# Kernel tuning notes

Measured on AMD Instinct MI355X. Metric: run time of the kernel, lower is better.

## Reference

```python
import jax, jax.numpy as jnp
import numpy as np

H = 512  # hidden_size


def _gru_gates(gi, gh, h):
    # gi, gh: [B, 3H] in PyTorch gate order (r, z, n)
    i_r, i_z, i_n = jnp.split(gi, 3, axis=-1)
    h_r, h_z, h_n = jnp.split(gh, 3, axis=-1)
    r = jax.nn.sigmoid(i_r + h_r)
    z = jax.nn.sigmoid(i_z + h_z)
    n = jnp.tanh(i_n + r * h_n)
    return (1.0 - z) * n + z * h


def _gru_layer(x, Wih, Whh, bih, bhh):
    # x: [B, T, in] -> outputs [B, T, H]; PyTorch nn.GRU math, h0 = 0
    gi = jnp.einsum('bti,gi->btg', x, Wih) + bih  # [B,T,3H], precompute input projections
    def step(h, gi_t):
        gh = h @ Whh.T + bhh
        h_new = _gru_gates(gi_t, gh, h)
        return h_new, h_new
    h0 = jnp.zeros((x.shape[0], H), dtype=x.dtype)
    _, hs = jax.lax.scan(step, h0, jnp.swapaxes(gi, 0, 1))
    return jnp.swapaxes(hs, 0, 1)


def _uniform_param(key, shape, fan):
    bound = 1.0 / np.sqrt(fan)
    return jax.random.uniform(key, shape, jnp.float32, -bound, bound)


def setup_inputs() -> dict:
    key = jax.random.key(0)
    ks = jax.random.split(key, 24)
    input_size, tf, B, T, horizon = 8, 8, 512, 336, 48
    inp = {
        'src': jax.random.normal(ks[0], (B, T, input_size), jnp.float32),
        'future_time_features': jax.random.normal(ks[1], (B, horizon, tf), jnp.float32),
        # encoder GRU layer 0
        'enc_Wih0': _uniform_param(ks[2], (3 * H, input_size), H),
        'enc_Whh0': _uniform_param(ks[3], (3 * H, H), H),
        'enc_bih0': _uniform_param(ks[4], (3 * H,), H),
        'enc_bhh0': _uniform_param(ks[5], (3 * H,), H),
        # encoder GRU layer 1
        'enc_Wih1': _uniform_param(ks[6], (3 * H, H), H),
        'enc_Whh1': _uniform_param(ks[7], (3 * H, H), H),
        'enc_bih1': _uniform_param(ks[8], (3 * H,), H),
        'enc_bhh1': _uniform_param(ks[9], (3 * H,), H),
        # dec0 Linear(H, H)
        'dec0_W': _uniform_param(ks[10], (H, H), H),
        'dec0_b': _uniform_param(ks[11], (H,), H),
        # decoder GRUCell(1 + tf, H)
        'cell_Wih': _uniform_param(ks[12], (3 * H, 1 + tf), H),
        'cell_Whh': _uniform_param(ks[13], (3 * H, H), H),
        'cell_bih': _uniform_param(ks[14], (3 * H,), H),
        'cell_bhh': _uniform_param(ks[15], (3 * H,), H),
        # fc Linear(H, 1)
        'fc_W': _uniform_param(ks[16], (1, H), H),
        'fc_b': _uniform_param(ks[17], (1,), H),
    }
    return inp


def reference(src, future_time_features,
              enc_Wih0, enc_Whh0, enc_bih0, enc_bhh0,
              enc_Wih1, enc_Whh1, enc_bih1, enc_bhh1,
              dec0_W, dec0_b, cell_Wih, cell_Whh, cell_bih, cell_bhh,
              fc_W, fc_b):
    # ---- encoder: 2-layer GRU, batch_first ----
    h1 = _gru_layer(src, enc_Wih0, enc_Whh0, enc_bih0, enc_bhh0)
    states = _gru_layer(h1, enc_Wih1, enc_Whh1, enc_bih1, enc_bhh1)  # [B,T,H]

    last_value = src[:, -1, 0:1]                      # [B,1]
    hidden = states[:, -1, :] @ dec0_W.T + dec0_b     # [B,H]

    tf_steps = jnp.swapaxes(future_time_features, 0, 1)  # [horizon,B,tf]

    def dec_step(carry, tf_t):
        hidden, last_value = carry
        x = jnp.concatenate([last_value, tf_t], axis=1)  # [B,1+tf]
        gi = x @ cell_Wih.T + cell_bih
        gh = hidden @ cell_Whh.T + cell_bhh
        hidden = _gru_gates(gi, gh, hidden)
        pred = hidden @ fc_W.T + fc_b                    # [B,1]
        return (hidden, pred), pred

    _, preds = jax.lax.scan(dec_step, (hidden, last_value), tf_steps)
    return jnp.swapaxes(preds, 0, 1)  # [B,horizon,1]
```

## Files before the change

### kernel.cpp

```cpp
#include <hip/hip_runtime.h>
#include <math.h>

typedef _Float16 half_t;
typedef _Float16 half8 __attribute__((ext_vector_type(8)));
typedef float floatx16 __attribute__((ext_vector_type(16)));
typedef unsigned int uint;

#define HD 512
#define BB 512
#define TT 336
#define HOR 48
#define NBLOCK 256
#define NTHREAD 512
#define GBLK 32
#define MFMA16(a,b,c) __builtin_amdgcn_mfma_f32_32x32x16_f16(a, b, c, 0, 0, 0)

__device__ __forceinline__ float sig_(float x) { return 1.0f / (1.0f + __expf(-x)); }

__global__ __launch_bounds__(256)
void prep_w2(const float* __restrict__ W1, const float* __restrict__ W2,
             half_t* __restrict__ D, int NKC, int NG)
{
    const int t = blockIdx.x * 256 + threadIdx.x;
    if (t >= 16 * NG * NKC * 64) return;
    const int lane = t & 63;
    const int kc = (t >> 6) % NKC;
    const int jtg = (t >> 6) / NKC;
    const int g = jtg % NG, jt = jtg / NG;
    const int row = g * 512 + jt * 32 + (lane & 31);
    const int k = kc * 16 + (lane >> 5) * 8;
    const float* Wp = (k < 512) ? W1 : W2;
    const int kk = (k < 512) ? k : (k - 512);
    const float4 lo = *(const float4*)(Wp + (size_t)row * 512 + kk);
    const float4 hi = *(const float4*)(Wp + (size_t)row * 512 + kk + 4);
    half8 h;
    h[0] = (half_t)lo.x; h[1] = (half_t)lo.y; h[2] = (half_t)lo.z; h[3] = (half_t)lo.w;
    h[4] = (half_t)hi.x; h[5] = (half_t)hi.y; h[6] = (half_t)hi.z; h[7] = (half_t)hi.w;
    *(half8*)(D + (size_t)t * 8) = h;
}

__global__ void lv_init_kernel(const float* __restrict__ src,
                               const float* __restrict__ fcb,
                               float* __restrict__ lvarr)
{
    const int b = threadIdx.x + blockIdx.x * blockDim.x;
    if (b < BB) lvarr[b] = src[((size_t)b * TT + (TT - 1)) * 8] - fcb[0];
}

struct PP {
    const half_t *BL0, *BWih1, *BWhh1, *Bcwhh, *Blin;
    half_t *h0f[2], *h1f[2], *hdf[2];
    float *hd32row;
    const float *src, *tff, *Wih0;
    const float *bih0, *bhh0, *bih1, *bhh1, *dec0b, *cWih, *cbih, *cbhh, *fcW, *fcb;
    float *lvarr, *out;
    uint *bars;
    int *tickets;
};

__device__ __forceinline__ uint aload_u(const uint* p) {
    return __hip_atomic_load(p, __ATOMIC_RELAXED, __HIP_MEMORY_SCOPE_AGENT);
}
__device__ __forceinline__ float aload_f(const float* p) {
    return __int_as_float(__hip_atomic_load((const int*)p, __ATOMIC_RELAXED, __HIP_MEMORY_SCOPE_AGENT));
}

__device__ __forceinline__ void xcd_barrier(uint* w)
{
    __syncthreads();
    if (threadIdx.x == 0) {
        const uint old = atomicAdd(w, 1u);
        const uint g0 = old >> 8;
        if ((old & 255u) == GBLK - 1) {
            __hip_atomic_store(w, (g0 + 1) << 8, __ATOMIC_RELAXED, __HIP_MEMORY_SCOPE_AGENT);
        } else {
            while ((aload_u(w) >> 8) == g0) __builtin_amdgcn_s_sleep(4);
        }
    }
    asm volatile("buffer_inv sc0" ::: "memory");
    __syncthreads();
}

__device__ __forceinline__ void dump_acc(float* red, int wv, int jl, int hi, const floatx16& a)
{
    #pragma unroll
    for (int rg = 0; rg < 16; ++rg)
        red[wv * 1024 + ((rg & 3) + 8 * (rg >> 2) + 4 * hi) * 32 + jl] = a[rg];
}
__device__ __forceinline__ void sum4(const float* red, int q, int jc, float* o)
{
    #pragma unroll
    for (int c = 0; c < 4; ++c) {
        const int ra = q * 4 + c, mi = ra >> 5, base = (ra & 31) * 32 + jc;
        o[c] = red[(0 + mi) * 1024 + base] + red[(2 + mi) * 1024 + base]
             + red[(4 + mi) * 1024 + base] + red[(6 + mi) * 1024 + base];
    }
}
__device__ __forceinline__ void sum22(const float* red, int q, int jc, float* lo, float* ho)
{
    #pragma unroll
    for (int c = 0; c < 4; ++c) {
        const int ra = q * 4 + c, mi = ra >> 5, base = (ra & 31) * 32 + jc;
        lo[c] = red[(0 + mi) * 1024 + base] + red[(2 + mi) * 1024 + base];
        ho[c] = red[(4 + mi) * 1024 + base] + red[(6 + mi) * 1024 + base];
    }
}

__device__ __forceinline__ void load_wlds(half_t* wlds, const half_t* Bsrc, int tid)
{
    #pragma unroll
    for (int it = 0; it < 12; ++it) {
        const int e = it * 512 + tid;
        const int gg = e >> 11, kc = (e >> 6) & 31, ln = e & 63;
        const int jj = ln & 31, h2 = ln >> 5;
        const half8 v = *(const half8*)(Bsrc + (size_t)e * 8);
        *(half8*)&wlds[(size_t)(gg * 32 + jj) * 512 + ((kc * 16 + h2 * 8) ^ ((jj & 15) << 3))] = v;
    }
}

__global__ __launch_bounds__(NTHREAD, 2)
void rnn_persist(PP p)
{
    __shared__ half_t wlds[3 * 32 * 512];
    __shared__ float  red[8 * 1024];
    __shared__ int    meta[2];
    __shared__ float  lvsh[64];

    const int tid = threadIdx.x;
    if (tid == 0) {
        int xcc;
        asm volatile("s_getreg_b32 %0, hwreg(HW_REG_XCC_ID)" : "=s"(xcc));
        xcc &= 7;
        meta[0] = xcc;
        meta[1] = atomicAdd(p.tickets + xcc, 1);
    }
    __syncthreads();
    const int g = meta[0];
    const int role = meta[1] & 31;
    const int L = role >> 4, jt = role & 15;

    const int wv = tid >> 6, lane = tid & 63;
    const int jl = lane & 31, hi = lane >> 5;
    const int mi = wv & 1, kh = wv >> 1;
    const int q = tid >> 5, jcell = tid & 31;
    const int row0g = g * 64;
    const int j = jt * 32 + jcell;
    const int swz16 = (jl & 15) << 3;
    const int gbase = g * 32768;
    const int joff = (j >> 4) * 512 + ((j >> 3) & 1) * 256 + (j & 7);

    uint* bword = p.bars + (size_t)g * 256;

    load_wlds(wlds, (L ? p.BWhh1 : p.BL0) + (size_t)jt * 6144 * 8, tid);

    const float* bi = L ? p.bih1 : p.bih0;
    const float* bh = L ? p.bhh1 : p.bhh0;
    const float bir = bi[j] + bh[j];
    const float biz = bi[512 + j] + bh[512 + j];
    const float bin = bi[1024 + j];
    const float bhn = bh[1024 + j];
    float w0r[8], w0z[8], w0n[8];
    if (!L) {
        #pragma unroll
        for (int i = 0; i < 8; ++i) {
            w0r[i] = p.Wih0[(size_t)j * 8 + i];
            w0z[i] = p.Wih0[(size_t)(512 + j) * 8 + i];
            w0n[i] = p.Wih0[(size_t)(1024 + j) * 8 + i];
        }
    }
    float hp[4] = {0.f, 0.f, 0.f, 0.f};

    for (int s = 0; s <= TT; ++s) {
        if (!L && s < TT) {
            floatx16 ar = {}, az = {}, an = {};
            const half_t* A = p.h0f[s & 1] + (size_t)(((g * 2 + mi) * 32 + kh * 8) * 64 + lane) * 8;
            #pragma unroll
            for (int kc = 0; kc < 8; ++kc) {
                const half8 a = *(const half8*)(A + kc * 512);
                const int ko = (kh * 128 + kc * 16 + hi * 8) ^ swz16;
                ar = MFMA16(a, *(const half8*)&wlds[(size_t)(0 * 32 + jl) * 512 + ko], ar);
                az = MFMA16(a, *(const half8*)&wlds[(size_t)(1 * 32 + jl) * 512 + ko], az);
                an = MFMA16(a, *(const half8*)&wlds[(size_t)(2 * 32 + jl) * 512 + ko], an);
            }
            float gr[4], gz[4], gn[4];
            dump_acc(red, wv, jl, hi, ar); __syncthreads(); sum4(red, q, jcell, gr); __syncthreads();
            dump_acc(red, wv, jl, hi, az); __syncthreads(); sum4(red, q, jcell, gz); __syncthreads();
            dump_acc(red, wv, jl, hi, an); __syncthreads(); sum4(red, q, jcell, gn);

            half_t* hofr = p.h0f[(s + 1) & 1];
            #pragma unroll
            for (int c = 0; c < 4; ++c) {
                const int r = q * 4 + c;
                const int br = row0g + r;
                const float* sp = p.src + ((size_t)br * TT + s) * 8;
                float xr = gr[c] + bir, xz = gz[c] + biz, xn = bin;
                #pragma unroll
                for (int i = 0; i < 8; ++i) {
                    const float xi = sp[i];
                    xr = fmaf(xi, w0r[i], xr);
                    xz = fmaf(xi, w0z[i], xz);
                    xn = fmaf(xi, w0n[i], xn);
                }
                const float rr = sig_(xr), zz = sig_(xz);
                const float nn = tanhf(xn + rr * (gn[c] + bhn));
                const float h = (1.f - zz) * nn + zz * hp[c];
                hp[c] = h;
                hofr[gbase + (r >> 5) * 16384 + (r & 31) * 8 + joff] = (half_t)h;
            }
        } else if (L && s >= 1) {
            floatx16 ar = {}, az = {}, an = {};
            if (kh < 2) {
                const half_t* A = p.h0f[s & 1] + (size_t)(((g * 2 + mi) * 32 + kh * 16) * 64 + lane) * 8;
                const half_t* Bb = p.BWih1 + ((size_t)jt * 6144 + kh * 1024 + lane) * 8;
                #pragma unroll 8
                for (int kc = 0; kc < 16; ++kc) {
                    const half8 a  = *(const half8*)(A + kc * 512);
                    const half8 u0 = *(const half8*)(Bb + (size_t)kc * 512);
                    const half8 u1 = *(const half8*)(Bb + (size_t)kc * 512 + 16384);
                    const half8 u2 = *(const half8*)(Bb + (size_t)kc * 512 + 32768);
                    ar = MFMA16(a, u0, ar);
                    az = MFMA16(a, u1, az);
                    an = MFMA16(a, u2, an);
                }
            } else {
                const half_t* A = p.h1f[s & 1] + (size_t)(((g * 2 + mi) * 32 + (kh - 2) * 16) * 64 + lane) * 8;
                #pragma unroll
                for (int kc = 0; kc < 16; ++kc) {
                    const half8 a = *(const half8*)(A + kc * 512);
                    const int ko = ((kh - 2) * 256 + kc * 16 + hi * 8) ^ swz16;
                    ar = MFMA16(a, *(const half8*)&wlds[(size_t)(0 * 32 + jl) * 512 + ko], ar);
                    az = MFMA16(a, *(const half8*)&wlds[(size_t)(1 * 32 + jl) * 512 + ko], az);
                    an = MFMA16(a, *(const half8*)&wlds[(size_t)(2 * 32 + jl) * 512 + ko], an);
                }
            }
            float gr[4], gz[4], gnl[4], gnh[4];
            dump_acc(red, wv, jl, hi, ar); __syncthreads(); sum4(red, q, jcell, gr); __syncthreads();
            dump_acc(red, wv, jl, hi, az); __syncthreads(); sum4(red, q, jcell, gz); __syncthreads();
            dump_acc(red, wv, jl, hi, an); __syncthreads(); sum22(red, q, jcell, gnl, gnh);

            half_t* hofr = p.h1f[(s + 1) & 1];
            #pragma unroll
            for (int c = 0; c < 4; ++c) {
                const int r = q * 4 + c;
                const float rr = sig_(gr[c] + bir), zz = sig_(gz[c] + biz);
                const float nn = tanhf(gnl[c] + bin + rr * (gnh[c] + bhn));
                const float h = (1.f - zz) * nn + zz * hp[c];
                hp[c] = h;
                hofr[gbase + (r >> 5) * 16384 + (r & 31) * 8 + joff] = (half_t)h;
            }
        }
        xcd_barrier(bword);
    }

    if (!L) {
        load_wlds(wlds, p.Bcwhh + (size_t)jt * 6144 * 8, tid);
    } else {
        floatx16 a0 = {};
        const half_t* A = p.h1f[1] + (size_t)(((g * 2 + mi) * 32 + kh * 8) * 64 + lane) * 8;
        const half_t* Bb = p.Blin + ((size_t)jt * 2048 + kh * 512 + lane) * 8;
        #pragma unroll
        for (int kc = 0; kc < 8; ++kc) {
            const half8 a = *(const half8*)(A + kc * 512);
            const half8 w = *(const half8*)(Bb + (size_t)kc * 512);
            a0 = MFMA16(a, w, a0);
        }
        float hv[4];
        dump_acc(red, wv, jl, hi, a0); __syncthreads(); sum4(red, q, jcell, hv);
        const float bj = p.dec0b[j];
        #pragma unroll
        for (int c = 0; c < 4; ++c) {
            const int r = q * 4 + c;
            const float h = hv[c] + bj;
            p.hd32row[(size_t)(row0g + r) * 512 + j] = h;
            p.hdf[0][gbase + (r >> 5) * 16384 + (r & 31) * 8 + joff] = (half_t)h;
        }
    }
    xcd_barrier(bword);

    float wR[9], wZ[9], wN[9];
    float dbr = 0.f, dbz = 0.f, dbn = 0.f, dbhn = 0.f, fw = 0.f, f0 = 0.f;
    if (!L) {
        #pragma unroll
        for (int i = 0; i < 9; ++i) {
            wR[i] = p.cWih[(size_t)j * 9 + i];
            wZ[i] = p.cWih[(size_t)(512 + j) * 9 + i];
            wN[i] = p.cWih[(size_t)(1024 + j) * 9 + i];
        }
        dbr = p.cbih[j] + p.cbhh[j];
        dbz = p.cbih[512 + j] + p.cbhh[512 + j];
        dbn = p.cbih[1024 + j];
        dbhn = p.cbhh[1024 + j];
        fw = p.fcW[j];
        f0 = p.fcb[0];
    }
    for (int s = 0; s < HOR; ++s) {
        if (!L && tid < 64)
            lvsh[tid] = aload_f(p.lvarr + (size_t)s * 512 + row0g + tid);
        __syncthreads();
        if (!L) {
            floatx16 ar = {}, az = {}, an = {};
            const half_t* A = p.hdf[s & 1] + (size_t)(((g * 2 + mi) * 32 + kh * 8) * 64 + lane) * 8;
            #pragma unroll
            for (int kc = 0; kc < 8; ++kc) {
                const half8 a = *(const half8*)(A + kc * 512);
                const int ko = (kh * 128 + kc * 16 + hi * 8) ^ swz16;
                ar = MFMA16(a, *(const half8*)&wlds[(size_t)(0 * 32 + jl) * 512 + ko], ar);
                az = MFMA16(a, *(const half8*)&wlds[(size_t)(1 * 32 + jl) * 512 + ko], az);
                an = MFMA16(a, *(const half8*)&wlds[(size_t)(2 * 32 + jl) * 512 + ko], an);
            }
            float gr[4], gz[4], gn[4];
            dump_acc(red, wv, jl, hi, ar); __syncthreads(); sum4(red, q, jcell, gr); __syncthreads();
            dump_acc(red, wv, jl, hi, az); __syncthreads(); sum4(red, q, jcell, gz); __syncthreads();
            dump_acc(red, wv, jl, hi, an); __syncthreads(); sum4(red, q, jcell, gn);

            half_t* hofr = p.hdf[(s + 1) & 1];
            #pragma unroll
            for (int c = 0; c < 4; ++c) {
                const int r = q * 4 + c;
                const int br = row0g + r;
                if (s == 0) hp[c] = p.hd32row[(size_t)br * 512 + j];
                const float x0 = lvsh[r] + f0;
                const float* sp = p.tff + ((size_t)br * HOR + s) * 8;
                float xr = gr[c] + dbr + x0 * wR[0];
                float xz = gz[c] + dbz + x0 * wZ[0];
                float xn = dbn + x0 * wN[0];
                #pragma unroll
                for (int i = 0; i < 8; ++i) {
                    const float xi = sp[i];
                    xr = fmaf(xi, wR[1 + i], xr);
                    xz = fmaf(xi, wZ[1 + i], xz);
                    xn = fmaf(xi, wN[1 + i], xn);
                }
                const float rr = sig_(xr), zz = sig_(xz);
                const float nn = tanhf(xn + rr * (gn[c] + dbhn));
                const float h = (1.f - zz) * nn + zz * hp[c];
                hp[c] = h;
                hofr[gbase + (r >> 5) * 16384 + (r & 31) * 8 + joff] = (half_t)h;

                float v = h * fw;
                #pragma unroll
                for (int off = 16; off > 0; off >>= 1) v += __shfl_xor(v, off);
                if (jl == 0 && (lane & 31) == 0) { }
                if ((lane & 31) == 0) {
                    atomicAdd(p.lvarr + (size_t)(s + 1) * 512 + br, v);
                    atomicAdd(p.out + (size_t)br * HOR + s, v + (role == 0 ? f0 : 0.f));
                }
            }
        }
        xcd_barrier(bword);
    }
}

extern "C" void kernel_launch(void* const* d_in, const int* in_sizes, int n_in,
                              void* d_out, int out_size, void* d_ws, size_t ws_size,
                              hipStream_t stream)
{
    const float* src   = (const float*)d_in[0];
    const float* tff   = (const float*)d_in[1];
    const float* Wih0  = (const float*)d_in[2];
    const float* Whh0  = (const float*)d_in[3];
    const float* bih0  = (const float*)d_in[4];
    const float* bhh0  = (const float*)d_in[5];
    const float* Wih1  = (const float*)d_in[6];
    const float* Whh1  = (const float*)d_in[7];
    const float* bih1  = (const float*)d_in[8];
    const float* bhh1  = (const float*)d_in[9];
    const float* dec0W = (const float*)d_in[10];
    const float* dec0b = (const float*)d_in[11];
    const float* cWih  = (const float*)d_in[12];
    const float* cWhh  = (const float*)d_in[13];
    const float* cbih  = (const float*)d_in[14];
    const float* cbhh  = (const float*)d_in[15];
    const float* fcW   = (const float*)d_in[16];
    const float* fcb   = (const float*)d_in[17];
    float* out = (float*)d_out;
    float* ws  = (float*)d_ws;

    constexpr size_t NFRAG = 131072;

    PP pp;
    size_t off = 0;
    pp.h0f[0] = (half_t*)(ws + off); off += NFRAG;
    pp.h1f[1] = (half_t*)(ws + off); off += NFRAG;
    pp.lvarr  = ws + off; off += (HOR + 1) * 512;
    pp.bars   = (uint*)(ws + off); off += 2048;
    pp.tickets = (int*)(ws + off); off += 64;
    const size_t zero_floats = off;
    pp.h0f[1] = (half_t*)(ws + off); off += NFRAG;
    pp.h1f[0] = (half_t*)(ws + off); off += NFRAG;
    pp.hdf[0] = (half_t*)(ws + off); off += NFRAG;
    pp.hdf[1] = (half_t*)(ws + off); off += NFRAG;
    pp.hd32row = ws + off; off += (size_t)BB * HD;
    half_t* BL0   = (half_t*)(ws + off); off += 393216;
    half_t* BWih1 = (half_t*)(ws + off); off += 393216;
    half_t* BWhh1 = (half_t*)(ws + off); off += 393216;
    half_t* Bcwhh = (half_t*)(ws + off); off += 393216;
    half_t* Blin  = (half_t*)(ws + off); off += 131072;

    pp.BL0 = BL0; pp.BWih1 = BWih1; pp.BWhh1 = BWhh1; pp.Bcwhh = Bcwhh; pp.Blin = Blin;
    pp.src = src; pp.tff = tff; pp.Wih0 = Wih0;
    pp.bih0 = bih0; pp.bhh0 = bhh0; pp.bih1 = bih1; pp.bhh1 = bhh1;
    pp.dec0b = dec0b; pp.cWih = cWih; pp.cbih = cbih; pp.cbhh = cbhh;
    pp.fcW = fcW; pp.fcb = fcb; pp.out = out;

    hipMemsetAsync(ws, 0, zero_floats * sizeof(float), stream);
    hipMemsetAsync(out, 0, (size_t)BB * HOR * sizeof(float), stream);
    prep_w2<<<384, 256, 0, stream>>>(Whh0, Whh0, BL0, 32, 3);
    prep_w2<<<384, 256, 0, stream>>>(Wih1, Wih1, BWih1, 32, 3);
    prep_w2<<<384, 256, 0, stream>>>(Whh1, Whh1, BWhh1, 32, 3);
    prep_w2<<<384, 256, 0, stream>>>(cWhh, cWhh, Bcwhh, 32, 3);
    prep_w2<<<128, 256, 0, stream>>>(dec0W, dec0W, Blin, 32, 1);
    lv_init_kernel<<<1, 512, 0, stream>>>(src, fcb, pp.lvarr);

    void* kargs[] = { (void*)&pp };
    hipLaunchCooperativeKernel((const void*)rnn_persist, dim3(NBLOCK), dim3(NTHREAD),
                               kargs, 0, stream);
}
```

Before: 2.879 ms.

## Replace atomic counter barrier with per-block flag slots and partial-sum buffers

Replaces the per-XCD atomic-add counter barrier with per-block monotonically increasing flag slots. Each block stores its own epoch, and 32 threads poll all peers' slots in parallel with a shorter sleep, which removes contention on a single atomic word. The decoder's last-value feedback also changes: atomicAdd into a shared array becomes plain stores of per-tile partial sums into a double-buffered buffer, and the next step sums those 16 partials. This cuts per-step atomic traffic and barrier latency on the serial recurrence, at the cost of more polling loads and a small reduction at each step.

```diff
diff --git a/kernel.cpp b/kernel.cpp
--- a/kernel.cpp
+++ b/kernel.cpp
@@ -41,10 +41,14 @@
 
 __global__ void lv_init_kernel(const float* __restrict__ src,
                                const float* __restrict__ fcb,
-                               float* __restrict__ lvarr)
+                               float* __restrict__ lvpart)
 {
     const int b = threadIdx.x + blockIdx.x * blockDim.x;
-    if (b < BB) lvarr[b] = src[((size_t)b * TT + (TT - 1)) * 8] - fcb[0];
+    if (b < BB) {
+        const int g = b >> 6, row = b & 63;
+        lvpart[((size_t)(g * 2 + 0) * 16 + 0) * 64 + row] =
+            src[((size_t)b * TT + (TT - 1)) * 8] - fcb[0];
+    }
 }
 
 struct PP {
@@ -53,29 +57,20 @@
     float *hd32row;
     const float *src, *tff, *Wih0;
     const float *bih0, *bhh0, *bih1, *bhh1, *dec0b, *cWih, *cbih, *cbhh, *fcW, *fcb;
-    float *lvarr, *out;
+    float *lvpart, *out;
     uint *bars;
     int *tickets;
 };
 
-__device__ __forceinline__ uint aload_u(const uint* p) {
-    return __hip_atomic_load(p, __ATOMIC_RELAXED, __HIP_MEMORY_SCOPE_AGENT);
-}
-__device__ __forceinline__ float aload_f(const float* p) {
-    return __int_as_float(__hip_atomic_load((const int*)p, __ATOMIC_RELAXED, __HIP_MEMORY_SCOPE_AGENT));
-}
-
-__device__ __forceinline__ void xcd_barrier(uint* w)
+__device__ __forceinline__ void xcd_barrier(uint* slots, int role, uint target)
 {
     __syncthreads();
-    if (threadIdx.x == 0) {
-        const uint old = atomicAdd(w, 1u);
-        const uint g0 = old >> 8;
-        if ((old & 255u) == GBLK - 1) {
-            __hip_atomic_store(w, (g0 + 1) << 8, __ATOMIC_RELAXED, __HIP_MEMORY_SCOPE_AGENT);
-        } else {
-            while ((aload_u(w) >> 8) == g0) __builtin_amdgcn_s_sleep(4);
-        }
+    if (threadIdx.x == 0)
+        __hip_atomic_store(slots + role * 16, target, __ATOMIC_RELAXED, __HIP_MEMORY_SCOPE_AGENT);
+    if (threadIdx.x < GBLK) {
+        while (__hip_atomic_load(slots + threadIdx.x * 16, __ATOMIC_RELAXED,
+                                 __HIP_MEMORY_SCOPE_AGENT) < target)
+            __builtin_amdgcn_s_sleep(1);
     }
     asm volatile("buffer_inv sc0" ::: "memory");
     __syncthreads();
@@ -149,7 +144,8 @@
     const int gbase = g * 32768;
     const int joff = (j >> 4) * 512 + ((j >> 3) & 1) * 256 + (j & 7);
 
-    uint* bword = p.bars + (size_t)g * 256;
+    uint* slots = p.bars + (size_t)g * GBLK * 16;
+    uint bcnt = 0;
 
     load_wlds(wlds, (L ? p.BWhh1 : p.BL0) + (size_t)jt * 6144 * 8, tid);
 
@@ -249,7 +245,7 @@
                 hofr[gbase + (r >> 5) * 16384 + (r & 31) * 8 + joff] = (half_t)h;
             }
         }
-        xcd_barrier(bword);
+        xcd_barrier(slots, role, ++bcnt);
     }
 
     if (!L) {
@@ -275,7 +271,7 @@
             p.hdf[0][gbase + (r >> 5) * 16384 + (r & 31) * 8 + joff] = (half_t)h;
         }
     }
-    xcd_barrier(bword);
+    xcd_barrier(slots, role, ++bcnt);
 
     float wR[9], wZ[9], wN[9];
     float dbr = 0.f, dbz = 0.f, dbn = 0.f, dbhn = 0.f, fw = 0.f, f0 = 0.f;
@@ -294,8 +290,13 @@
         f0 = p.fcb[0];
     }
     for (int s = 0; s < HOR; ++s) {
-        if (!L && tid < 64)
-            lvsh[tid] = aload_f(p.lvarr + (size_t)s * 512 + row0g + tid);
+        if (!L && tid < 64) {
+            const float* lp = p.lvpart + ((size_t)(g * 2 + (s & 1)) * 16) * 64 + tid;
+            float acc = 0.f;
+            #pragma unroll
+            for (int rr = 0; rr < 16; ++rr) acc += lp[rr * 64];
+            lvsh[tid] = acc;
+        }
         __syncthreads();
         if (!L) {
             floatx16 ar = {}, az = {}, an = {};
@@ -340,14 +341,13 @@
                 float v = h * fw;
                 #pragma unroll
                 for (int off = 16; off > 0; off >>= 1) v += __shfl_xor(v, off);
-                if (jl == 0 && (lane & 31) == 0) { }
                 if ((lane & 31) == 0) {
-                    atomicAdd(p.lvarr + (size_t)(s + 1) * 512 + br, v);
+                    p.lvpart[((size_t)(g * 2 + ((s + 1) & 1)) * 16 + jt) * 64 + r] = v;
                     atomicAdd(p.out + (size_t)br * HOR + s, v + (role == 0 ? f0 : 0.f));
                 }
             }
         }
-        xcd_barrier(bword);
+        xcd_barrier(slots, role, ++bcnt);
     }
 }
 
@@ -382,8 +382,8 @@
     size_t off = 0;
     pp.h0f[0] = (half_t*)(ws + off); off += NFRAG;
     pp.h1f[1] = (half_t*)(ws + off); off += NFRAG;
-    pp.lvarr  = ws + off; off += (HOR + 1) * 512;
-    pp.bars   = (uint*)(ws + off); off += 2048;
+    pp.lvpart = ws + off; off += 8 * 2 * 16 * 64;
+    pp.bars   = (uint*)(ws + off); off += 8 * GBLK * 16;
     pp.tickets = (int*)(ws + off); off += 64;
     const size_t zero_floats = off;
     pp.h0f[1] = (half_t*)(ws + off); off += NFRAG;
@@ -410,7 +410,7 @@
     prep_w2<<<384, 256, 0, stream>>>(Whh1, Whh1, BWhh1, 32, 3);
     prep_w2<<<384, 256, 0, stream>>>(cWhh, cWhh, Bcwhh, 32, 3);
     prep_w2<<<128, 256, 0, stream>>>(dec0W, dec0W, Blin, 32, 1);
-    lv_init_kernel<<<1, 512, 0, stream>>>(src, fcb, pp.lvarr);
+    lv_init_kernel<<<1, 512, 0, stream>>>(src, fcb, pp.lvpart);
 
     void* kargs[] = { (void*)&pp };
     hipLaunchCooperativeKernel((const void*)rnn_persist, dim3(NBLOCK), dim3(NTHREAD),
```

Measured after the change: 3.224 ms. 1.12x slower.
